# Performance work log

Hardware: AMD Instinct MI355X
Metric: run time of the kernel (lower is better)

Reference implementation:

```python
import jax, jax.numpy as jnp
import numpy as np


def _sepconv1x1(x, dw, pw, b):
    # SeparableConv2D with kernel=1: depthwise 1x1 = per-channel scale, then pointwise matmul
    return jnp.einsum('nhwc,cd->nhwd', x * dw, pw) + b


def setup_inputs() -> dict:
    key = jax.random.key(0)
    ks = jax.random.split(key, 12)
    N, H, W, C_in, C_red = 4, 64, 64, 256, 64
    s = 0.05  # small init so softmax logits are well-conditioned
    return {
        'feature_maps': jax.random.normal(ks[0], (N, H, W, C_in), jnp.float32),
        'global_channel_output': jax.random.normal(ks[1], (N, H, W, C_in), jnp.float32),
        'dw_q': jax.random.normal(ks[2], (C_in,), jnp.float32) * s,
        'pw_q': jax.random.normal(ks[3], (C_in, C_red), jnp.float32) * s,
        'b_q': jnp.zeros((C_red,), jnp.float32),
        'dw_k': jax.random.normal(ks[4], (C_in,), jnp.float32) * s,
        'pw_k': jax.random.normal(ks[5], (C_in, C_red), jnp.float32) * s,
        'b_k': jnp.zeros((C_red,), jnp.float32),
        'dw_v': jax.random.normal(ks[6], (C_in,), jnp.float32) * s,
        'pw_v': jax.random.normal(ks[7], (C_in, C_red), jnp.float32) * s,
        'b_v': jnp.zeros((C_red,), jnp.float32),
        'dw_a': jax.random.normal(ks[8], (C_red,), jnp.float32) * s,
        'pw_a': jax.random.normal(ks[9], (C_red, C_in), jnp.float32) * s,
        'b_a': jnp.zeros((C_in,), jnp.float32),
    }


def reference(feature_maps, global_channel_output,
              dw_q, pw_q, b_q, dw_k, pw_k, b_k, dw_v, pw_v, b_v,
              dw_a, pw_a, b_a):
    N, H, W, _ = feature_maps.shape
    q = _sepconv1x1(feature_maps, dw_q, pw_q, b_q)  # [N,H,W,Cr]
    k = _sepconv1x1(feature_maps, dw_k, pw_k, b_k)
    v = _sepconv1x1(feature_maps, dw_v, pw_v, b_v)
    Cr = q.shape[-1]
    q = q.reshape(N, H * W, Cr)
    k = k.reshape(N, H * W, Cr)
    v = v.reshape(N, H * W, Cr)
    # tf.matmul(key, query, transpose_b=True): scores[i,j] = key_i . query_j
    scores = jnp.einsum('nic,njc->nij', k, q)  # [N,HW,HW]
    scores = jax.nn.softmax(scores, axis=-1)
    # tf.matmul(value, scores, transpose_a=True) -> [N,Cr,HW]
    att = jnp.einsum('nic,nij->ncj', v, scores)
    # faithful raw reshape (as in the original TF code) from [N,Cr,HW] to [N,H,W,Cr]
    att = att.reshape(N, H, W, Cr)
    att = _sepconv1x1(att, dw_a, pw_a, b_a)  # [N,H,W,C_in]
    return global_channel_output * att + global_channel_output
```

## Files before the change

kernel.cpp:

```cpp
#include <hip/hip_runtime.h>
#include <hip/hip_bf16.h>

typedef __attribute__((ext_vector_type(8))) __bf16 bf16x8;
typedef __attribute__((ext_vector_type(2))) __bf16 bf16x2;
typedef __attribute__((ext_vector_type(4))) float floatx4;
typedef __attribute__((ext_vector_type(4))) unsigned short us4;
typedef __attribute__((ext_vector_type(8))) unsigned short us8;
typedef __attribute__((ext_vector_type(4))) short s16x4;
typedef __attribute__((ext_vector_type(2))) unsigned int uint2v;
typedef __attribute__((ext_vector_type(4))) unsigned int uint4v;

#define MFMA16(A, B, C) __builtin_amdgcn_mfma_f32_16x16x32_bf16((A), (B), (C), 0, 0, 0)
#define MFMA1K(A, B, C) __builtin_amdgcn_mfma_f32_16x16x16bf16_1k((A), (B), (C), 0, 0, 0)

#define LOG2E 1.44269504088896340736f

#if __has_builtin(__builtin_amdgcn_exp2f)
#define EXP2F(x) __builtin_amdgcn_exp2f(x)
#else
#define EXP2F(x) exp2f(x)
#endif

static __device__ __forceinline__ unsigned short f2bfbits(float f) {
    __hip_bfloat16 h = __float2bfloat16(f);
    union { __hip_bfloat16 h; unsigned short u; } cv;
    cv.h = h;
    return cv.u;
}
static __device__ __forceinline__ unsigned int rne32(float f) {
    unsigned int u = __builtin_bit_cast(unsigned int, f);
    return u + 0x7fffu + ((u >> 16) & 1u);
}
static __device__ __forceinline__ unsigned short rne16(float f) {
    return (unsigned short)(rne32(f) >> 16);
}

#if __has_builtin(__builtin_amdgcn_cvt_pk_bf16_f32)
static __device__ __forceinline__ s16x4 pack4(float e0, float e1, float e2, float e3) {
    bf16x2 lo = __builtin_amdgcn_cvt_pk_bf16_f32(e0, e1);
    bf16x2 hi = __builtin_amdgcn_cvt_pk_bf16_f32(e2, e3);
    uint2v u = {__builtin_bit_cast(unsigned int, lo), __builtin_bit_cast(unsigned int, hi)};
    return __builtin_bit_cast(s16x4, u);
}
static __device__ __forceinline__ bf16x8 cvt8(floatx4 a, floatx4 b) {
    bf16x2 p0 = __builtin_amdgcn_cvt_pk_bf16_f32(a[0], a[1]);
    bf16x2 p1 = __builtin_amdgcn_cvt_pk_bf16_f32(a[2], a[3]);
    bf16x2 p2 = __builtin_amdgcn_cvt_pk_bf16_f32(b[0], b[1]);
    bf16x2 p3 = __builtin_amdgcn_cvt_pk_bf16_f32(b[2], b[3]);
    uint4v u = {__builtin_bit_cast(unsigned int, p0), __builtin_bit_cast(unsigned int, p1),
                __builtin_bit_cast(unsigned int, p2), __builtin_bit_cast(unsigned int, p3)};
    return __builtin_bit_cast(bf16x8, u);
}
#else
static __device__ __forceinline__ s16x4 pack4(float e0, float e1, float e2, float e3) {
    unsigned int pa = __builtin_amdgcn_perm(rne32(e1), rne32(e0), 0x07060302u);
    unsigned int pb = __builtin_amdgcn_perm(rne32(e3), rne32(e2), 0x07060302u);
    uint2v u = {pa, pb};
    return __builtin_bit_cast(s16x4, u);
}
static __device__ __forceinline__ bf16x8 cvt8(floatx4 a, floatx4 b) {
    us8 u;
#pragma unroll
    for (int i = 0; i < 4; i++) { u[i] = rne16(a[i]); u[4 + i] = rne16(b[i]); }
    return __builtin_bit_cast(bf16x8, u);
}
#endif

static __device__ __forceinline__ bf16x8 load_bf8(const __hip_bfloat16* p) {
    return *reinterpret_cast<const bf16x8*>(p);
}
static __device__ __forceinline__ float bf2f(unsigned short u) {
    unsigned int w = ((unsigned int)u) << 16;
    return __builtin_bit_cast(float, w);
}


__global__ __launch_bounds__(256) void prep_w(
    const float* __restrict__ dwq, const float* __restrict__ pwq,
    const float* __restrict__ dwk, const float* __restrict__ pwk,
    const float* __restrict__ dwv, const float* __restrict__ pwv,
    __hip_bfloat16* __restrict__ wT)
{
    int idx = blockIdx.x * 256 + threadIdx.x;
    int p = idx >> 14;
    int r = idx & 16383;
    int d = r >> 8, c = r & 255;
    const float* dw = (p == 0) ? dwq : ((p == 1) ? dwk : dwv);
    const float* pw = (p == 0) ? pwq : ((p == 1) ? pwk : pwv);
    float scale = (p == 1) ? LOG2E : 1.0f;
    wT[idx] = __float2bfloat16(dw[c] * pw[c * 64 + d] * scale);
}

__global__ __launch_bounds__(256) void proj_qkv(
    const float* __restrict__ x,
    const __hip_bfloat16* __restrict__ wT,
    const float* __restrict__ bqp, const float* __restrict__ bkp,
    const float* __restrict__ bvp,
    __hip_bfloat16* __restrict__ qf, __hip_bfloat16* __restrict__ kf,
    __hip_bfloat16* __restrict__ vf)
{
    int wg = blockIdx.x * 4 + (threadIdx.x >> 6);
    int p = wg >> 10;
    int wid = wg & 1023;
    int lane = threadIdx.x & 63;
    int l15 = lane & 15, quad = lane >> 4;
    int strip = wid << 4;

    floatx4 acc[4];
#pragma unroll
    for (int t = 0; t < 4; t++) acc[t] = (floatx4){0.f, 0.f, 0.f, 0.f};

    const float* xrow = x + (strip + l15) * 256 + quad * 8;
    const __hip_bfloat16* wp = wT + p * 16384;
#pragma unroll
    for (int ks = 0; ks < 8; ks++) {
        floatx4 xa = *reinterpret_cast<const floatx4*>(xrow + ks * 32);
        floatx4 xb = *reinterpret_cast<const floatx4*>(xrow + ks * 32 + 4);
        bf16x8 a = cvt8(xa, xb);
#pragma unroll
        for (int t = 0; t < 4; t++) {
            bf16x8 b = load_bf8(wp + (t * 16 + l15) * 256 + ks * 32 + quad * 8);
            acc[t] = MFMA16(a, b, acc[t]);
        }
    }
    if (p < 2) {
        __hip_bfloat16* dst = (p == 0) ? qf : kf;
        const float* bias = (p == 0) ? bqp : bkp;
        float bscale = (p == 1) ? LOG2E : 1.0f;
#pragma unroll
        for (int t = 0; t < 4; t++) {
            float bsv = bias[t * 16 + l15] * bscale;
            int off0 = wid * 1024 + (t >> 1) * 512 +
                       (((((t & 1) << 1) | (l15 >> 3)) * 16 + quad * 4) * 8) + (l15 & 7);
#pragma unroll
            for (int r = 0; r < 4; r++)
                dst[off0 + r * 8] = __float2bfloat16(acc[t][r] + bsv);
        }
    } else {
#pragma unroll
        for (int t = 0; t < 4; t++) {
            float bsv = bvp[t * 16 + l15];
            us4 pk;
#pragma unroll
            for (int r = 0; r < 4; r++) pk[r] = f2bfbits(acc[t][r] + bsv);
            *reinterpret_cast<us4*>(vf + (wid * 4 + t) * 256 + lane * 4) = pk;
        }
    }
}

__global__ __launch_bounds__(512) void pass1_rl(
    const __hip_bfloat16* __restrict__ qf, const __hip_bfloat16* __restrict__ kf,
    const __hip_bfloat16* __restrict__ vf, __hip_bfloat16* __restrict__ vfs)
{
    int itg0 = blockIdx.x * 2;
    int n = itg0 >> 8;
    int jw = threadIdx.x >> 6;
    int lane = threadIdx.x & 63;
    int l15 = lane & 15, quad = lane >> 4;

    const __hip_bfloat16* kp = kf + itg0 * 1024 + lane * 8;
    bf16x8 a0 = load_bf8(kp);
    bf16x8 a1 = load_bf8(kp + 512);
    bf16x8 a2 = load_bf8(kp + 1024);
    bf16x8 a3 = load_bf8(kp + 1536);

    floatx4 lsA = (floatx4){0.f, 0.f, 0.f, 0.f};
    floatx4 lsB = (floatx4){0.f, 0.f, 0.f, 0.f};
    const __hip_bfloat16* qp0 = qf + (n * 256 + jw * 32) * 1024 + lane * 8;
    for (int it = 0; it < 16; it++, qp0 += 2048) {
        bf16x8 b0 = load_bf8(qp0);
        bf16x8 b1 = load_bf8(qp0 + 512);
        bf16x8 b2 = load_bf8(qp0 + 1024);
        bf16x8 b3 = load_bf8(qp0 + 1536);
        floatx4 z = (floatx4){0.f, 0.f, 0.f, 0.f};
        floatx4 sA0 = MFMA16(a1, b1, MFMA16(a0, b0, z));
        floatx4 sA1 = MFMA16(a1, b3, MFMA16(a0, b2, z));
        floatx4 sB0 = MFMA16(a3, b1, MFMA16(a2, b0, z));
        floatx4 sB1 = MFMA16(a3, b3, MFMA16(a2, b2, z));
#pragma unroll
        for (int r = 0; r < 4; r++) {
            lsA[r] += EXP2F(sA0[r]) + EXP2F(sA1[r]);
            lsB[r] += EXP2F(sB0[r]) + EXP2F(sB1[r]);
        }
    }
#pragma unroll
    for (int m = 1; m < 16; m <<= 1) {
#pragma unroll
        for (int r = 0; r < 4; r++) {
            lsA[r] += __shfl_xor(lsA[r], m, 64);
            lsB[r] += __shfl_xor(lsB[r], m, 64);
        }
    }
    __shared__ float red[8][32];
    __shared__ float rls[32];
    if (l15 == 0) {
#pragma unroll
        for (int r = 0; r < 4; r++) {
            red[jw][quad * 4 + r] = lsA[r];
            red[jw][16 + quad * 4 + r] = lsB[r];
        }
    }
    __syncthreads();
    if (threadIdx.x < 32) {
        float tot = 0.f;
#pragma unroll
        for (int w = 0; w < 8; w++) tot += red[w][threadIdx.x];
        rls[threadIdx.x] = 1.0f / tot;
    }
    __syncthreads();
    int m0 = threadIdx.x * 4;
    int toff = m0 >> 10;
    int mm = m0 & 1023;
    int rb = toff * 16 + ((mm >> 6) & 3) * 4;
    const unsigned short* vin = reinterpret_cast<const unsigned short*>(vf) + itg0 * 1024 + m0;
    us4 vv = *reinterpret_cast<const us4*>(vin);
    us4 ov;
#pragma unroll
    for (int r = 0; r < 4; r++) ov[r] = rne16(bf2f(vv[r]) * rls[rb + r]);
    *reinterpret_cast<us4*>(reinterpret_cast<unsigned short*>(vfs) + itg0 * 1024 + m0) = ov;
}

__global__ __launch_bounds__(256) void pass2_att(
    const __hip_bfloat16* __restrict__ qf, const __hip_bfloat16* __restrict__ kf,
    const __hip_bfloat16* __restrict__ vfs,
    unsigned short* __restrict__ attp)
{
    int b = blockIdx.x;
    int ih = b & 7;
    int g = b >> 3;
    int n = g >> 5;
    int jg = g & 31;
    int w = threadIdx.x >> 6;
    int jt0 = jg * 8 + w * 2;
    int lane = threadIdx.x & 63;
    int l15 = lane & 15, quad = lane >> 4;

    const __hip_bfloat16* qp = qf + (n * 256 + jt0) * 1024 + lane * 8;
    bf16x8 bq00 = load_bf8(qp);
    bf16x8 bq01 = load_bf8(qp + 512);
    bf16x8 bq10 = load_bf8(qp + 1024);
    bf16x8 bq11 = load_bf8(qp + 1536);

    floatx4 acc0[4], acc1[4];
#pragma unroll
    for (int t = 0; t < 4; t++) {
        acc0[t] = (floatx4){0.f, 0.f, 0.f, 0.f};
        acc1[t] = (floatx4){0.f, 0.f, 0.f, 0.f};
    }

    int it0 = n * 256 + ih * 32;
    const __hip_bfloat16* kp = kf + it0 * 1024 + lane * 8;
    const __hip_bfloat16* vp = vfs + it0 * 1024;
    for (int it = 0; it < 32; it++, kp += 1024, vp += 1024) {
        bf16x8 a0 = load_bf8(kp);
        bf16x8 a1 = load_bf8(kp + 512);
        floatx4 z = (floatx4){0.f, 0.f, 0.f, 0.f};
        floatx4 s0a = MFMA16(a0, bq00, z);
        floatx4 s0b = MFMA16(a1, bq01, z);
        floatx4 s1a = MFMA16(a0, bq10, z);
        floatx4 s1b = MFMA16(a1, bq11, z);
        floatx4 s0 = s0a + s0b;
        floatx4 s1 = s1a + s1b;
        s16x4 p0 = pack4(EXP2F(s0[0]), EXP2F(s0[1]), EXP2F(s0[2]), EXP2F(s0[3]));
        s16x4 p1 = pack4(EXP2F(s1[0]), EXP2F(s1[1]), EXP2F(s1[2]), EXP2F(s1[3]));
#pragma unroll
        for (int t = 0; t < 4; t++) {
            s16x4 bv = *reinterpret_cast<const s16x4*>(vp + t * 256 + lane * 4);
            acc0[t] = MFMA1K(p0, bv, acc0[t]);
            acc1[t] = MFMA1K(p1, bv, acc1[t]);
        }
    }
    unsigned short* op0 = attp + ih * 1048576;
#pragma unroll
    for (int t = 0; t < 4; t++) {
        s16x4 k0 = pack4(acc0[t][0], acc0[t][1], acc0[t][2], acc0[t][3]);
        s16x4 k1 = pack4(acc1[t][0], acc1[t][1], acc1[t][2], acc1[t][3]);
        unsigned short* op = op0 + (n * 64 + t * 16 + l15) * 4096 + jt0 * 16 + quad * 4;
        *reinterpret_cast<s16x4*>(op) = k0;
        *reinterpret_cast<s16x4*>(op + 16) = k1;
    }
}

__global__ __launch_bounds__(256) void final_out(
    const unsigned short* __restrict__ attp, const float* __restrict__ gco,
    const float* __restrict__ dwa, const float* __restrict__ pwa,
    const float* __restrict__ ba, float* __restrict__ out)
{
    int b = blockIdx.x;
    int n = b >> 9;
    int hh = (b >> 3) & 63;
    int w0 = (b & 7) << 3;
    __shared__ float g[512];
    int tid = threadIdx.x;
    const unsigned short* ap = attp + (n * 64 + hh) * 4096 + w0 * 64;
    for (int jj = tid; jj < 512; jj += 256) {
        float v = 0.f;
#pragma unroll
        for (int ph = 0; ph < 8; ph++) v += bf2f(ap[ph * 1048576 + jj]);
        g[jj] = v * dwa[jj & 63];
    }
    __syncthreads();
    float acc[8];
#pragma unroll
    for (int w = 0; w < 8; w++) acc[w] = 0.f;
    for (int cc = 0; cc < 64; cc++) {
        float p = pwa[cc * 256 + tid];
#pragma unroll
        for (int w = 0; w < 8; w++) acc[w] += g[w * 64 + cc] * p;
    }
    float bb = ba[tid];
#pragma unroll
    for (int w = 0; w < 8; w++) {
        int pos = (n * 64 + hh) * 64 + w0 + w;
        float gv = gco[pos * 256 + tid];
        out[pos * 256 + tid] = gv * (acc[w] + bb) + gv;
    }
}

extern "C" void kernel_launch(void* const* d_in, const int* in_sizes, int n_in,
                              void* d_out, int out_size, void* d_ws, size_t ws_size,
                              hipStream_t stream) {
    const float* x   = (const float*)d_in[0];
    const float* gco = (const float*)d_in[1];
    const float* dwq = (const float*)d_in[2];
    const float* pwq = (const float*)d_in[3];
    const float* bq  = (const float*)d_in[4];
    const float* dwk = (const float*)d_in[5];
    const float* pwk = (const float*)d_in[6];
    const float* bk  = (const float*)d_in[7];
    const float* dwv = (const float*)d_in[8];
    const float* pwv = (const float*)d_in[9];
    const float* bv  = (const float*)d_in[10];
    const float* dwa = (const float*)d_in[11];
    const float* pwa = (const float*)d_in[12];
    const float* ba  = (const float*)d_in[13];
    float* out = (float*)d_out;

    char* ws = (char*)d_ws;
    __hip_bfloat16* wT  = (__hip_bfloat16*)ws;
    __hip_bfloat16* qf  = (__hip_bfloat16*)(ws + 98304);
    __hip_bfloat16* kf  = (__hip_bfloat16*)(ws + 2195456);
    __hip_bfloat16* vf  = (__hip_bfloat16*)(ws + 4292608);
    __hip_bfloat16* vfs = (__hip_bfloat16*)(ws + 6389760);
    unsigned short* attp = (unsigned short*)(ws + 8486912);

    prep_w<<<192, 256, 0, stream>>>(dwq, pwq, dwk, pwk, dwv, pwv, wT);
    proj_qkv<<<768, 256, 0, stream>>>(x, wT, bq, bk, bv, qf, kf, vf);
    pass1_rl<<<512, 512, 0, stream>>>(qf, kf, vf, vfs);
    pass2_att<<<1024, 256, 0, stream>>>(qf, kf, vfs, attp);
    final_out<<<2048, 256, 0, stream>>>(attp, gco, dwa, pwa, ba, out);
}
```

Baseline: 181.1 us.

## Split attention key range finer, halve pass1 tiles, and repack V for wide loads

pass1 now handles one 16-row key tile per block, doubling the grid, and writes the rescaled V in a lane-interleaved layout. pass2 reads each lane's V fragment with two 16-byte loads instead of four 8-byte loads. When the workspace is large enough, pass2 splits the key range into 16 partitions instead of 8 to raise parallelism, and final_out sums 16 partial results. The trade-off is more partial-output traffic and a heavier reduction step in final_out.

```diff
diff --git a/kernel.cpp b/kernel.cpp
--- a/kernel.cpp
+++ b/kernel.cpp
@@ -148,24 +148,21 @@
     }
 }
 
-__global__ __launch_bounds__(512) void pass1_rl(
+__global__ __launch_bounds__(512, 8) void pass1_rl(
     const __hip_bfloat16* __restrict__ qf, const __hip_bfloat16* __restrict__ kf,
     const __hip_bfloat16* __restrict__ vf, __hip_bfloat16* __restrict__ vfs)
 {
-    int itg0 = blockIdx.x * 2;
-    int n = itg0 >> 8;
+    int itg = blockIdx.x;
+    int n = itg >> 8;
     int jw = threadIdx.x >> 6;
     int lane = threadIdx.x & 63;
     int l15 = lane & 15, quad = lane >> 4;
 
-    const __hip_bfloat16* kp = kf + itg0 * 1024 + lane * 8;
+    const __hip_bfloat16* kp = kf + itg * 1024 + lane * 8;
     bf16x8 a0 = load_bf8(kp);
     bf16x8 a1 = load_bf8(kp + 512);
-    bf16x8 a2 = load_bf8(kp + 1024);
-    bf16x8 a3 = load_bf8(kp + 1536);
-
-    floatx4 lsA = (floatx4){0.f, 0.f, 0.f, 0.f};
-    floatx4 lsB = (floatx4){0.f, 0.f, 0.f, 0.f};
+
+    floatx4 ls = (floatx4){0.f, 0.f, 0.f, 0.f};
     const __hip_bfloat16* qp0 = qf + (n * 256 + jw * 32) * 1024 + lane * 8;
     for (int it = 0; it < 16; it++, qp0 += 2048) {
         bf16x8 b0 = load_bf8(qp0);
@@ -175,59 +172,51 @@
         floatx4 z = (floatx4){0.f, 0.f, 0.f, 0.f};
         floatx4 sA0 = MFMA16(a1, b1, MFMA16(a0, b0, z));
         floatx4 sA1 = MFMA16(a1, b3, MFMA16(a0, b2, z));
-        floatx4 sB0 = MFMA16(a3, b1, MFMA16(a2, b0, z));
-        floatx4 sB1 = MFMA16(a3, b3, MFMA16(a2, b2, z));
-#pragma unroll
-        for (int r = 0; r < 4; r++) {
-            lsA[r] += EXP2F(sA0[r]) + EXP2F(sA1[r]);
-            lsB[r] += EXP2F(sB0[r]) + EXP2F(sB1[r]);
-        }
+#pragma unroll
+        for (int r = 0; r < 4; r++) ls[r] += EXP2F(sA0[r]) + EXP2F(sA1[r]);
     }
 #pragma unroll
     for (int m = 1; m < 16; m <<= 1) {
 #pragma unroll
-        for (int r = 0; r < 4; r++) {
-            lsA[r] += __shfl_xor(lsA[r], m, 64);
-            lsB[r] += __shfl_xor(lsB[r], m, 64);
-        }
-    }
-    __shared__ float red[8][32];
-    __shared__ float rls[32];
+        for (int r = 0; r < 4; r++) ls[r] += __shfl_xor(ls[r], m, 64);
+    }
+    __shared__ float red[8][16];
+    __shared__ float rls[16];
     if (l15 == 0) {
 #pragma unroll
-        for (int r = 0; r < 4; r++) {
-            red[jw][quad * 4 + r] = lsA[r];
-            red[jw][16 + quad * 4 + r] = lsB[r];
-        }
+        for (int r = 0; r < 4; r++) red[jw][quad * 4 + r] = ls[r];
     }
     __syncthreads();
-    if (threadIdx.x < 32) {
+    if (threadIdx.x < 16) {
         float tot = 0.f;
 #pragma unroll
         for (int w = 0; w < 8; w++) tot += red[w][threadIdx.x];
         rls[threadIdx.x] = 1.0f / tot;
     }
     __syncthreads();
-    int m0 = threadIdx.x * 4;
-    int toff = m0 >> 10;
-    int mm = m0 & 1023;
-    int rb = toff * 16 + ((mm >> 6) & 3) * 4;
-    const unsigned short* vin = reinterpret_cast<const unsigned short*>(vf) + itg0 * 1024 + m0;
-    us4 vv = *reinterpret_cast<const us4*>(vin);
-    us4 ov;
-#pragma unroll
-    for (int r = 0; r < 4; r++) ov[r] = rne16(bf2f(vv[r]) * rls[rb + r]);
-    *reinterpret_cast<us4*>(reinterpret_cast<unsigned short*>(vfs) + itg0 * 1024 + m0) = ov;
-}
-
-__global__ __launch_bounds__(256) void pass2_att(
+    int m0 = threadIdx.x * 2;
+    int t = m0 >> 8;
+    int l = (m0 >> 2) & 63;
+    int e0 = m0 & 3;
+    int q2 = l >> 4;
+    unsigned int vv = *reinterpret_cast<const unsigned int*>(
+        reinterpret_cast<const unsigned short*>(vf) + itg * 1024 + m0);
+    float f0 = bf2f((unsigned short)(vv & 0xffffu)) * rls[q2 * 4 + e0];
+    float f1 = bf2f((unsigned short)(vv >> 16)) * rls[q2 * 4 + e0 + 1];
+    unsigned int ov = (rne32(f0) >> 16) | (rne32(f1) & 0xffff0000u);
+    *reinterpret_cast<unsigned int*>(
+        reinterpret_cast<unsigned short*>(vfs) + itg * 1024 + l * 16 + t * 4 + e0) = ov;
+}
+
+template<int ITERS, int IHB>
+__global__ __launch_bounds__(256, 8) void pass2_att(
     const __hip_bfloat16* __restrict__ qf, const __hip_bfloat16* __restrict__ kf,
     const __hip_bfloat16* __restrict__ vfs,
     unsigned short* __restrict__ attp)
 {
     int b = blockIdx.x;
-    int ih = b & 7;
-    int g = b >> 3;
+    int ih = b & ((1 << IHB) - 1);
+    int g = b >> IHB;
     int n = g >> 5;
     int jg = g & 31;
     int w = threadIdx.x >> 6;
@@ -248,27 +237,31 @@
         acc1[t] = (floatx4){0.f, 0.f, 0.f, 0.f};
     }
 
-    int it0 = n * 256 + ih * 32;
+    int it0 = n * 256 + ih * ITERS;
     const __hip_bfloat16* kp = kf + it0 * 1024 + lane * 8;
-    const __hip_bfloat16* vp = vfs + it0 * 1024;
-    for (int it = 0; it < 32; it++, kp += 1024, vp += 1024) {
+    const __hip_bfloat16* vp = vfs + it0 * 1024 + lane * 16;
+    for (int it = 0; it < ITERS; it++, kp += 1024, vp += 1024) {
         bf16x8 a0 = load_bf8(kp);
         bf16x8 a1 = load_bf8(kp + 512);
         floatx4 z = (floatx4){0.f, 0.f, 0.f, 0.f};
-        floatx4 s0a = MFMA16(a0, bq00, z);
-        floatx4 s0b = MFMA16(a1, bq01, z);
-        floatx4 s1a = MFMA16(a0, bq10, z);
-        floatx4 s1b = MFMA16(a1, bq11, z);
-        floatx4 s0 = s0a + s0b;
-        floatx4 s1 = s1a + s1b;
+        floatx4 s0 = MFMA16(a1, bq01, MFMA16(a0, bq00, z));
+        floatx4 s1 = MFMA16(a1, bq11, MFMA16(a0, bq10, z));
         s16x4 p0 = pack4(EXP2F(s0[0]), EXP2F(s0[1]), EXP2F(s0[2]), EXP2F(s0[3]));
         s16x4 p1 = pack4(EXP2F(s1[0]), EXP2F(s1[1]), EXP2F(s1[2]), EXP2F(s1[3]));
-#pragma unroll
-        for (int t = 0; t < 4; t++) {
-            s16x4 bv = *reinterpret_cast<const s16x4*>(vp + t * 256 + lane * 4);
-            acc0[t] = MFMA1K(p0, bv, acc0[t]);
-            acc1[t] = MFMA1K(p1, bv, acc1[t]);
-        }
+        us8 v01 = *reinterpret_cast<const us8*>(vp);
+        us8 v23 = *reinterpret_cast<const us8*>(vp + 8);
+        s16x4 bv0 = __builtin_bit_cast(s16x4, __builtin_shufflevector(v01, v01, 0, 1, 2, 3));
+        s16x4 bv1 = __builtin_bit_cast(s16x4, __builtin_shufflevector(v01, v01, 4, 5, 6, 7));
+        s16x4 bv2 = __builtin_bit_cast(s16x4, __builtin_shufflevector(v23, v23, 0, 1, 2, 3));
+        s16x4 bv3 = __builtin_bit_cast(s16x4, __builtin_shufflevector(v23, v23, 4, 5, 6, 7));
+        acc0[0] = MFMA1K(p0, bv0, acc0[0]);
+        acc1[0] = MFMA1K(p1, bv0, acc1[0]);
+        acc0[1] = MFMA1K(p0, bv1, acc0[1]);
+        acc1[1] = MFMA1K(p1, bv1, acc1[1]);
+        acc0[2] = MFMA1K(p0, bv2, acc0[2]);
+        acc1[2] = MFMA1K(p1, bv2, acc1[2]);
+        acc0[3] = MFMA1K(p0, bv3, acc0[3]);
+        acc1[3] = MFMA1K(p1, bv3, acc1[3]);
     }
     unsigned short* op0 = attp + ih * 1048576;
 #pragma unroll
@@ -281,6 +274,7 @@
     }
 }
 
+template<int NPART>
 __global__ __launch_bounds__(256) void final_out(
     const unsigned short* __restrict__ attp, const float* __restrict__ gco,
     const float* __restrict__ dwa, const float* __restrict__ pwa,
@@ -296,7 +290,7 @@
     for (int jj = tid; jj < 512; jj += 256) {
         float v = 0.f;
 #pragma unroll
-        for (int ph = 0; ph < 8; ph++) v += bf2f(ap[ph * 1048576 + jj]);
+        for (int ph = 0; ph < NPART; ph++) v += bf2f(ap[ph * 1048576 + jj]);
         g[jj] = v * dwa[jj & 63];
     }
     __syncthreads();
@@ -344,9 +338,16 @@
     __hip_bfloat16* vfs = (__hip_bfloat16*)(ws + 6389760);
     unsigned short* attp = (unsigned short*)(ws + 8486912);
 
+    const size_t NEED16 = 8486912u + 16u * 2097152u;
+
     prep_w<<<192, 256, 0, stream>>>(dwq, pwq, dwk, pwk, dwv, pwv, wT);
     proj_qkv<<<768, 256, 0, stream>>>(x, wT, bq, bk, bv, qf, kf, vf);
-    pass1_rl<<<512, 512, 0, stream>>>(qf, kf, vf, vfs);
-    pass2_att<<<1024, 256, 0, stream>>>(qf, kf, vfs, attp);
-    final_out<<<2048, 256, 0, stream>>>(attp, gco, dwa, pwa, ba, out);
-}
+    pass1_rl<<<1024, 512, 0, stream>>>(qf, kf, vf, vfs);
+    if (ws_size >= NEED16) {
+        pass2_att<16, 4><<<2048, 256, 0, stream>>>(qf, kf, vfs, attp);
+        final_out<16><<<2048, 256, 0, stream>>>(attp, gco, dwa, pwa, ba, out);
+    } else {
+        pass2_att<32, 3><<<1024, 256, 0, stream>>>(qf, kf, vfs, attp);
+        final_out<8><<<2048, 256, 0, stream>>>(attp, gco, dwa, pwa, ba, out);
+    }
+}
```

Result: slower. 298.6 us (+64.9%).

## Split attention key range finer, relayout scaled V for wide loads

Applied to the files above, without the earlier changes.

The scaled V written by pass1 is stored in a new interleaved layout, so each lane in pass2 reads its four 4-element B fragments with two 16-byte loads instead of four 8-byte loads. pass2 is templated on the number of key tiles per block, and when the workspace is large enough it uses 16 partitions with 2048 blocks instead of 8 with 1024, giving more parallelism. final_out sums the matching number of partials with paired 32-bit loads. The score MFMAs are also chained through the accumulator instead of being added afterwards. The cost is more partial-sum traffic and a larger workspace, and the choice depends on the workspace size at runtime.

```diff
diff --git a/kernel.cpp b/kernel.cpp
--- a/kernel.cpp
+++ b/kernel.cpp
@@ -211,23 +211,27 @@
     int m0 = threadIdx.x * 4;
     int toff = m0 >> 10;
     int mm = m0 & 1023;
-    int rb = toff * 16 + ((mm >> 6) & 3) * 4;
-    const unsigned short* vin = reinterpret_cast<const unsigned short*>(vf) + itg0 * 1024 + m0;
-    us4 vv = *reinterpret_cast<const us4*>(vin);
+    int t = mm >> 8;
+    int l = (mm >> 2) & 63;
+    int rb = toff * 16 + (l >> 4) * 4;
+    us4 vv = *reinterpret_cast<const us4*>(
+        reinterpret_cast<const unsigned short*>(vf) + itg0 * 1024 + m0);
     us4 ov;
 #pragma unroll
     for (int r = 0; r < 4; r++) ov[r] = rne16(bf2f(vv[r]) * rls[rb + r]);
-    *reinterpret_cast<us4*>(reinterpret_cast<unsigned short*>(vfs) + itg0 * 1024 + m0) = ov;
-}
-
+    *reinterpret_cast<us4*>(
+        reinterpret_cast<unsigned short*>(vfs) + (itg0 + toff) * 1024 + l * 16 + t * 4) = ov;
+}
+
+template<int ITERS, int IHB>
 __global__ __launch_bounds__(256) void pass2_att(
     const __hip_bfloat16* __restrict__ qf, const __hip_bfloat16* __restrict__ kf,
     const __hip_bfloat16* __restrict__ vfs,
     unsigned short* __restrict__ attp)
 {
     int b = blockIdx.x;
-    int ih = b & 7;
-    int g = b >> 3;
+    int ih = b & ((1 << IHB) - 1);
+    int g = b >> IHB;
     int n = g >> 5;
     int jg = g & 31;
     int w = threadIdx.x >> 6;
@@ -248,27 +252,31 @@
         acc1[t] = (floatx4){0.f, 0.f, 0.f, 0.f};
     }
 
-    int it0 = n * 256 + ih * 32;
+    int it0 = n * 256 + ih * ITERS;
     const __hip_bfloat16* kp = kf + it0 * 1024 + lane * 8;
-    const __hip_bfloat16* vp = vfs + it0 * 1024;
-    for (int it = 0; it < 32; it++, kp += 1024, vp += 1024) {
+    const __hip_bfloat16* vp = vfs + it0 * 1024 + lane * 16;
+    for (int it = 0; it < ITERS; it++, kp += 1024, vp += 1024) {
         bf16x8 a0 = load_bf8(kp);
         bf16x8 a1 = load_bf8(kp + 512);
         floatx4 z = (floatx4){0.f, 0.f, 0.f, 0.f};
-        floatx4 s0a = MFMA16(a0, bq00, z);
-        floatx4 s0b = MFMA16(a1, bq01, z);
-        floatx4 s1a = MFMA16(a0, bq10, z);
-        floatx4 s1b = MFMA16(a1, bq11, z);
-        floatx4 s0 = s0a + s0b;
-        floatx4 s1 = s1a + s1b;
+        floatx4 s0 = MFMA16(a1, bq01, MFMA16(a0, bq00, z));
+        floatx4 s1 = MFMA16(a1, bq11, MFMA16(a0, bq10, z));
         s16x4 p0 = pack4(EXP2F(s0[0]), EXP2F(s0[1]), EXP2F(s0[2]), EXP2F(s0[3]));
         s16x4 p1 = pack4(EXP2F(s1[0]), EXP2F(s1[1]), EXP2F(s1[2]), EXP2F(s1[3]));
-#pragma unroll
-        for (int t = 0; t < 4; t++) {
-            s16x4 bv = *reinterpret_cast<const s16x4*>(vp + t * 256 + lane * 4);
-            acc0[t] = MFMA1K(p0, bv, acc0[t]);
-            acc1[t] = MFMA1K(p1, bv, acc1[t]);
-        }
+        us8 v01 = *reinterpret_cast<const us8*>(vp);
+        us8 v23 = *reinterpret_cast<const us8*>(vp + 8);
+        s16x4 bv0 = __builtin_bit_cast(s16x4, __builtin_shufflevector(v01, v01, 0, 1, 2, 3));
+        s16x4 bv1 = __builtin_bit_cast(s16x4, __builtin_shufflevector(v01, v01, 4, 5, 6, 7));
+        s16x4 bv2 = __builtin_bit_cast(s16x4, __builtin_shufflevector(v23, v23, 0, 1, 2, 3));
+        s16x4 bv3 = __builtin_bit_cast(s16x4, __builtin_shufflevector(v23, v23, 4, 5, 6, 7));
+        acc0[0] = MFMA1K(p0, bv0, acc0[0]);
+        acc1[0] = MFMA1K(p1, bv0, acc1[0]);
+        acc0[1] = MFMA1K(p0, bv1, acc0[1]);
+        acc1[1] = MFMA1K(p1, bv1, acc1[1]);
+        acc0[2] = MFMA1K(p0, bv2, acc0[2]);
+        acc1[2] = MFMA1K(p1, bv2, acc1[2]);
+        acc0[3] = MFMA1K(p0, bv3, acc0[3]);
+        acc1[3] = MFMA1K(p1, bv3, acc1[3]);
     }
     unsigned short* op0 = attp + ih * 1048576;
 #pragma unroll
@@ -281,6 +289,7 @@
     }
 }
 
+template<int NPART>
 __global__ __launch_bounds__(256) void final_out(
     const unsigned short* __restrict__ attp, const float* __restrict__ gco,
     const float* __restrict__ dwa, const float* __restrict__ pwa,
@@ -293,11 +302,17 @@
     __shared__ float g[512];
     int tid = threadIdx.x;
     const unsigned short* ap = attp + (n * 64 + hh) * 4096 + w0 * 64;
-    for (int jj = tid; jj < 512; jj += 256) {
-        float v = 0.f;
-#pragma unroll
-        for (int ph = 0; ph < 8; ph++) v += bf2f(ap[ph * 1048576 + jj]);
-        g[jj] = v * dwa[jj & 63];
+    {
+        int jj0 = tid * 2;
+        float v0 = 0.f, v1 = 0.f;
+#pragma unroll
+        for (int ph = 0; ph < NPART; ph++) {
+            unsigned int u = *reinterpret_cast<const unsigned int*>(ap + ph * 1048576 + jj0);
+            v0 += bf2f((unsigned short)(u & 0xffffu));
+            v1 += bf2f((unsigned short)(u >> 16));
+        }
+        g[jj0] = v0 * dwa[jj0 & 63];
+        g[jj0 + 1] = v1 * dwa[(jj0 + 1) & 63];
     }
     __syncthreads();
     float acc[8];
@@ -344,9 +359,16 @@
     __hip_bfloat16* vfs = (__hip_bfloat16*)(ws + 6389760);
     unsigned short* attp = (unsigned short*)(ws + 8486912);
 
+    const size_t NEED16 = 8486912u + 16u * 2097152u;
+
     prep_w<<<192, 256, 0, stream>>>(dwq, pwq, dwk, pwk, dwv, pwv, wT);
     proj_qkv<<<768, 256, 0, stream>>>(x, wT, bq, bk, bv, qf, kf, vf);
     pass1_rl<<<512, 512, 0, stream>>>(qf, kf, vf, vfs);
-    pass2_att<<<1024, 256, 0, stream>>>(qf, kf, vfs, attp);
-    final_out<<<2048, 256, 0, stream>>>(attp, gco, dwa, pwa, ba, out);
-}
+    if (ws_size >= NEED16) {
+        pass2_att<16, 4><<<2048, 256, 0, stream>>>(qf, kf, vfs, attp);
+        final_out<16><<<2048, 256, 0, stream>>>(attp, gco, dwa, pwa, ba, out);
+    } else {
+        pass2_att<32, 3><<<1024, 256, 0, stream>>>(qf, kf, vfs, attp);
+        final_out<8><<<2048, 256, 0, stream>>>(attp, gco, dwa, pwa, ba, out);
+    }
+}
```

Measured after the change: 182.6 us. Within noise of the previous version (+0.8%).
